# Performance work log

Hardware: AMD Instinct MI355X
Metric: run time of the kernel (lower is better)

Reference implementation:

```python
import jax, jax.numpy as jnp
import numpy as np

B, C, W, H = 8, 256, 64, 64


def _conv1x1(x, w, b):
    # 1x1 conv == per-pixel channel GEMM. x: [B,C,W,H], w: [O,C], b: [O]
    return jnp.einsum('oc,bchw->bohw', w, x) + b[None, :, None, None]


def setup_inputs() -> dict:
    key = jax.random.key(0)
    ks = jax.random.split(key, 9)
    s = 1.0 / np.sqrt(C)
    return {
        'queries': jax.random.normal(ks[0], (B, C, W, H), dtype=jnp.float32),
        'keys': jax.random.normal(ks[1], (B, C, W, H), dtype=jnp.float32),
        'mask': jax.random.uniform(ks[2], (B, 1, W, H), dtype=jnp.float32),
        'Wq': jax.random.normal(ks[3], (C, C), dtype=jnp.float32) * s,
        'bq': jax.random.normal(ks[4], (C,), dtype=jnp.float32) * 0.01,
        'Wk': jax.random.normal(ks[5], (C, C), dtype=jnp.float32) * s,
        'bk': jax.random.normal(ks[6], (C,), dtype=jnp.float32) * 0.01,
        'Wv': jax.random.normal(ks[7], (C, C), dtype=jnp.float32) * s,
        'bv': jax.random.normal(ks[8], (C,), dtype=jnp.float32) * 0.01,
    }


def reference(queries, keys, mask, Wq, bq, Wk, bk, Wv, bv):
    b, c, w, h = queries.shape
    n = w * h
    q = _conv1x1(queries, Wq, bq).reshape(b, c, n)   # [B,C,N]
    k = _conv1x1(keys, Wk, bk).reshape(b, c, n)      # [B,C,N]
    v = _conv1x1(keys, Wv, bv).reshape(b, c, n)      # [B,C,N]
    # mask spatial size equals feature size -> interpolate(scale_factor=1) is identity
    m = mask.reshape(b, n)                            # [B,N]
    # scores[b,i,j] = <q_i, k_j>; torch's repeated mask multiplies row i by mask[i]
    scores = jnp.einsum('bcq,bck->bqk', q, k) * m[:, :, None]
    attn_w = jax.nn.softmax(scores, axis=-1)          # softmax over key dim
    attn = jnp.einsum('bqk,bck->bcq', attn_w, v).reshape(b, c, w, h)
    return queries * mask + (1.0 - mask) * attn
```

## Files before the change

### kernel.cpp

```cpp
#include <hip/hip_runtime.h>

typedef __attribute__((ext_vector_type(8))) _Float16 half8;
typedef __attribute__((ext_vector_type(4))) _Float16 half4;
typedef __attribute__((ext_vector_type(4))) float f32x4;

#define CDIM 256
#define NDIM 4096
#define MFMAH(a, b, c) __builtin_amdgcn_mfma_f32_16x16x32_f16((a), (b), (c), 0, 0, 0)

#define GLOAD_LDS16(gp, lp)                                              \
  __builtin_amdgcn_global_load_lds(                                      \
      (const __attribute__((address_space(1))) void*)(gp),               \
      (__attribute__((address_space(3))) void*)(lp), 16, 0, 0)

__global__ void cast_w_kernel(const float* __restrict__ Wq,
                              const float* __restrict__ Wk,
                              const float* __restrict__ Wv,
                              _Float16* __restrict__ Wc) {
  int t = blockIdx.x * 256 + threadIdx.x;
  int mat = t >> 14;
  int idx = (t & 16383) * 4;
  const float* W = (mat == 0) ? Wq : (mat == 1 ? Wk : Wv);
  float4 w = *(const float4*)(W + idx);
  half4 h = {(_Float16)w.x, (_Float16)w.y, (_Float16)w.z, (_Float16)w.w};
  *(half4*)(Wc + mat * 65536 + idx) = h;
}

__global__ __launch_bounds__(256, 2) void proj_kernel(
    const float* __restrict__ queries, const float* __restrict__ keys,
    const _Float16* __restrict__ Wc,
    const float* __restrict__ bq, const float* __restrict__ bk,
    const float* __restrict__ bv,
    _Float16* __restrict__ Qh, _Float16* __restrict__ Kh,
    _Float16* __restrict__ Vh)
{
  const int z = blockIdx.z, p = z >> 3, b = z & 7;
  const float* __restrict__ X = (p == 0) ? queries : keys;
  const _Float16* __restrict__ W = Wc + p * 65536;
  const float* __restrict__ bias = (p == 0) ? bq : (p == 1 ? bk : bv);
  const int n0 = blockIdx.x * 128;

  __shared__ __align__(16) _Float16 Xs[128][264];

  const int tid = threadIdx.x;
  const int wv = tid >> 6, lane = tid & 63, l16 = lane & 15, quad = lane >> 4;

#pragma unroll
  for (int it = 0; it < 32; ++it) {
    int id = tid + it * 256;
    int c = id >> 5, n4 = id & 31;
    float4 x = *(const float4*)&X[((size_t)(b * CDIM + c)) * NDIM + n0 + n4 * 4];
    Xs[n4 * 4 + 0][c] = (_Float16)x.x;
    Xs[n4 * 4 + 1][c] = (_Float16)x.y;
    Xs[n4 * 4 + 2][c] = (_Float16)x.z;
    Xs[n4 * 4 + 3][c] = (_Float16)x.w;
  }
  __syncthreads();

  f32x4 acc[4][8];
#pragma unroll
  for (int og = 0; og < 4; ++og)
#pragma unroll
    for (int ng = 0; ng < 8; ++ng) acc[og][ng] = (f32x4){0.f, 0.f, 0.f, 0.f};

#pragma unroll
  for (int kc = 0; kc < 8; ++kc) {
    half8 wf[4], xf[8];
#pragma unroll
    for (int og = 0; og < 4; ++og)
      wf[og] = *(const half8*)(W + (wv * 64 + og * 16 + l16) * CDIM + kc * 32 + quad * 8);
#pragma unroll
    for (int ng = 0; ng < 8; ++ng)
      xf[ng] = *(const half8*)&Xs[ng * 16 + l16][kc * 32 + quad * 8];
#pragma unroll
    for (int og = 0; og < 4; ++og)
#pragma unroll
      for (int ng = 0; ng < 8; ++ng)
        acc[og][ng] = MFMAH(wf[og], xf[ng], acc[og][ng]);
  }

#pragma unroll
  for (int og = 0; og < 4; ++og) {
    float4 b4 = *(const float4*)&bias[wv * 64 + og * 16 + quad * 4];
#pragma unroll
    for (int ng = 0; ng < 8; ++ng) {
      const int n = n0 + ng * 16 + l16;
      if (p == 2) {
#pragma unroll
        for (int r = 0; r < 4; ++r) {
          int o = wv * 64 + og * 16 + quad * 4 + r;
          float y = acc[og][ng][r] + ((const float*)&b4)[r];
          Vh[((size_t)(b * CDIM + o)) * NDIM + n] = (_Float16)y;
        }
      } else {
        half4 h4;
#pragma unroll
        for (int r = 0; r < 4; ++r)
          h4[r] = (_Float16)(acc[og][ng][r] + ((const float*)&b4)[r]);
        size_t idx = ((size_t)(b * NDIM + n)) * CDIM + wv * 64 + og * 16 + quad * 4;
        if (p == 0) *(half4*)&Qh[idx] = h4;
        else        *(half4*)&Kh[idx] = h4;
      }
    }
  }
}

__global__ __launch_bounds__(256, 2) void attn_kernel(
    const float* __restrict__ queries, const float* __restrict__ mask,
    const _Float16* __restrict__ Qh, const _Float16* __restrict__ Kh,
    const _Float16* __restrict__ Vh, float* __restrict__ out)
{
  const int blk = blockIdx.x, b = blk & 7, it = blk >> 3;
  const int i0 = it * 64;

  __shared__ __align__(16) _Float16 Ks[64 * 256];
  __shared__ __align__(16) _Float16 Ps[2][64][88];
  __shared__ __align__(16) float Al[2][64];
  __shared__ __align__(16) float Li[64];

  const int tid = threadIdx.x;
  const int wv = tid >> 6, lane = tid & 63, l16 = lane & 15, quad = lane >> 4;

  const float LOG2E = 1.44269504088896f;

  half8 qf[8];
  {
    const size_t qrow = ((size_t)(b * NDIM + i0 + wv * 16 + l16)) * CDIM;
#pragma unroll
    for (int kc = 0; kc < 8; ++kc)
      qf[kc] = *(const half8*)(Qh + qrow + kc * 32 + quad * 8);
  }
  const float mvalL = mask[(size_t)b * NDIM + i0 + wv * 16 + l16] * LOG2E;
  float m_run = -1e30f, l_run = 0.f;

  f32x4 O[4][4];
#pragma unroll
  for (int g = 0; g < 4; ++g)
#pragma unroll
    for (int cg = 0; cg < 4; ++cg) O[g][cg] = (f32x4){0.f, 0.f, 0.f, 0.f};

  const _Float16* __restrict__ Kb = Kh + (size_t)b * NDIM * CDIM;
  const _Float16* __restrict__ Vw = Vh + ((size_t)(b * CDIM + wv * 64)) * NDIM;

  const int jrow = tid >> 5;
  const int scol = ((tid & 31) * 8) ^ ((jrow & 7) << 3);
  char* const ldst0 = (char*)Ks + (size_t)tid * 16;
  const int kswz = (l16 & 7) << 3;

#pragma unroll
  for (int st = 0; st < 8; ++st)
    GLOAD_LDS16(Kb + (size_t)(st * 8 + jrow) * CDIM + scol, ldst0 + st * 4096);

  for (int jt = 0; jt < 64; ++jt) {
    const int j0 = jt * 64;
    const int pb = jt & 1;
    half8 vf[2][4];
#pragma unroll
    for (int kk = 0; kk < 2; ++kk)
#pragma unroll
      for (int cg = 0; cg < 4; ++cg)
        vf[kk][cg] = *(const half8*)(Vw + (size_t)(cg * 16 + l16) * NDIM + j0 + kk * 32 + quad * 8);
    __syncthreads();

    f32x4 s[4];
#pragma unroll
    for (int js = 0; js < 4; ++js) s[js] = (f32x4){0.f, 0.f, 0.f, 0.f};
#pragma unroll
    for (int kc = 0; kc < 8; ++kc) {
#pragma unroll
      for (int js = 0; js < 4; ++js) {
        half8 kf = *(const half8*)&Ks[(js * 16 + l16) * 256 + ((kc * 32 + quad * 8) ^ kswz)];
        s[js] = MFMAH(kf, qf[kc], s[js]);
      }
    }

    float a[16];
    float mx = -1e30f;
#pragma unroll
    for (int js = 0; js < 4; ++js)
#pragma unroll
      for (int r = 0; r < 4; ++r) {
        float v = s[js][r] * mvalL;
        a[js * 4 + r] = v;
        mx = fmaxf(mx, v);
      }
    mx = fmaxf(mx, __shfl_xor(mx, 16));
    mx = fmaxf(mx, __shfl_xor(mx, 32));
    const float mnew = fmaxf(m_run, mx);
    const float alpha = exp2f(m_run - mnew);
    m_run = mnew;
    float psum = 0.f;
#pragma unroll
    for (int js = 0; js < 4; ++js) {
      float p0 = exp2f(a[js * 4 + 0] - mnew);
      float p1 = exp2f(a[js * 4 + 1] - mnew);
      float p2 = exp2f(a[js * 4 + 2] - mnew);
      float p3 = exp2f(a[js * 4 + 3] - mnew);
      psum += (p0 + p1) + (p2 + p3);
      half4 hp = {(_Float16)p0, (_Float16)p1, (_Float16)p2, (_Float16)p3};
      *(half4*)&Ps[pb][wv * 16 + l16][js * 16 + quad * 4] = hp;
    }
    psum += __shfl_xor(psum, 16);
    psum += __shfl_xor(psum, 32);
    l_run = l_run * alpha + psum;
    if (quad == 0) Al[pb][wv * 16 + l16] = alpha;
    __syncthreads();

    if (jt < 63) {
      const _Float16* srcn = Kb + (size_t)((jt + 1) * 64 + jrow) * CDIM + scol;
#pragma unroll
      for (int st = 0; st < 8; ++st)
        GLOAD_LDS16(srcn + (size_t)st * 8 * CDIM, ldst0 + st * 4096);
    }

    f32x4 av[4];
#pragma unroll
    for (int g = 0; g < 4; ++g) av[g] = *(const f32x4*)&Al[pb][g * 16 + quad * 4];
#pragma unroll
    for (int g = 0; g < 4; ++g)
#pragma unroll
      for (int cg = 0; cg < 4; ++cg)
#pragma unroll
        for (int r = 0; r < 4; ++r) O[g][cg][r] *= av[g][r];
#pragma unroll
    for (int kk = 0; kk < 2; ++kk) {
      half8 pa[4];
#pragma unroll
      for (int g = 0; g < 4; ++g)
        pa[g] = *(const half8*)&Ps[pb][g * 16 + l16][kk * 32 + quad * 8];
#pragma unroll
      for (int g = 0; g < 4; ++g)
#pragma unroll
        for (int cg = 0; cg < 4; ++cg)
          O[g][cg] = MFMAH(pa[g], vf[kk][cg], O[g][cg]);
    }
  }

  if (quad == 0) Li[wv * 16 + l16] = 1.0f / l_run;
  __syncthreads();
#pragma unroll
  for (int g = 0; g < 4; ++g) {
    f32x4 li4 = *(const f32x4*)&Li[g * 16 + quad * 4];
    const int i = i0 + g * 16 + quad * 4;
    float4 m4 = *(const float4*)&mask[(size_t)b * NDIM + i];
#pragma unroll
    for (int cg = 0; cg < 4; ++cg) {
      const int c = wv * 64 + cg * 16 + l16;
      const size_t base = ((size_t)(b * CDIM + c)) * NDIM + i;
      float4 q4 = *(const float4*)(queries + base);
      float4 o4;
      o4.x = q4.x * m4.x + (1.f - m4.x) * (O[g][cg][0] * li4[0]);
      o4.y = q4.y * m4.y + (1.f - m4.y) * (O[g][cg][1] * li4[1]);
      o4.z = q4.z * m4.z + (1.f - m4.z) * (O[g][cg][2] * li4[2]);
      o4.w = q4.w * m4.w + (1.f - m4.w) * (O[g][cg][3] * li4[3]);
      *(float4*)(out + base) = o4;
    }
  }
}

extern "C" void kernel_launch(void* const* d_in, const int* in_sizes, int n_in,
                              void* d_out, int out_size, void* d_ws, size_t ws_size,
                              hipStream_t stream) {
  const float* queries = (const float*)d_in[0];
  const float* keys    = (const float*)d_in[1];
  const float* mask    = (const float*)d_in[2];
  const float* Wq = (const float*)d_in[3];
  const float* bq = (const float*)d_in[4];
  const float* Wk = (const float*)d_in[5];
  const float* bk = (const float*)d_in[6];
  const float* Wv = (const float*)d_in[7];
  const float* bv = (const float*)d_in[8];
  float* out = (float*)d_out;

  const size_t elems = (size_t)8 * NDIM * CDIM;
  _Float16* Qh = (_Float16*)d_ws;
  _Float16* Kh = Qh + elems;
  _Float16* Vh = Kh + elems;
  _Float16* Wc = Vh + elems;

  cast_w_kernel<<<dim3(192), 256, 0, stream>>>(Wq, Wk, Wv, Wc);
  proj_kernel<<<dim3(32, 1, 24), 256, 0, stream>>>(
      queries, keys, Wc, bq, bk, bv, Qh, Kh, Vh);
  attn_kernel<<<dim3(512), 256, 0, stream>>>(
      queries, mask, Qh, Kh, Vh, out);
}
```

Before: 327.5 us.

## Split projection tile into two halves and prefetch second half into registers

The projection kernel now processes its 128-column tile as two 64-column halves. The second half's input is loaded into registers while the first half's MFMAs and stores run, then converted and written to a second LDS buffer. This is meant to overlap global-load latency with compute and to halve the accumulator register footprint. In exchange, each thread holds 16 float4 prefetch registers and the W fragments are reloaded for each half.

```diff
diff --git a/kernel.cpp b/kernel.cpp
--- a/kernel.cpp
+++ b/kernel.cpp
@@ -40,67 +40,91 @@
   const float* __restrict__ bias = (p == 0) ? bq : (p == 1 ? bk : bv);
   const int n0 = blockIdx.x * 128;
 
-  __shared__ __align__(16) _Float16 Xs[128][264];
+  __shared__ __align__(16) _Float16 Xs[2][64][264];
 
   const int tid = threadIdx.x;
   const int wv = tid >> 6, lane = tid & 63, l16 = lane & 15, quad = lane >> 4;
 
 #pragma unroll
-  for (int it = 0; it < 32; ++it) {
+  for (int it = 0; it < 16; ++it) {
     int id = tid + it * 256;
-    int c = id >> 5, n4 = id & 31;
+    int c = id >> 4, n4 = id & 15;
     float4 x = *(const float4*)&X[((size_t)(b * CDIM + c)) * NDIM + n0 + n4 * 4];
-    Xs[n4 * 4 + 0][c] = (_Float16)x.x;
-    Xs[n4 * 4 + 1][c] = (_Float16)x.y;
-    Xs[n4 * 4 + 2][c] = (_Float16)x.z;
-    Xs[n4 * 4 + 3][c] = (_Float16)x.w;
+    Xs[0][n4 * 4 + 0][c] = (_Float16)x.x;
+    Xs[0][n4 * 4 + 1][c] = (_Float16)x.y;
+    Xs[0][n4 * 4 + 2][c] = (_Float16)x.z;
+    Xs[0][n4 * 4 + 3][c] = (_Float16)x.w;
   }
   __syncthreads();
 
-  f32x4 acc[4][8];
-#pragma unroll
-  for (int og = 0; og < 4; ++og)
-#pragma unroll
-    for (int ng = 0; ng < 8; ++ng) acc[og][ng] = (f32x4){0.f, 0.f, 0.f, 0.f};
-
-#pragma unroll
-  for (int kc = 0; kc < 8; ++kc) {
-    half8 wf[4], xf[8];
+  float4 xs1[16];
+#pragma unroll
+  for (int it = 0; it < 16; ++it) {
+    int id = tid + it * 256;
+    int c = id >> 4, n4 = id & 15;
+    xs1[it] = *(const float4*)&X[((size_t)(b * CDIM + c)) * NDIM + n0 + 64 + n4 * 4];
+  }
+
+#pragma unroll
+  for (int s = 0; s < 2; ++s) {
+    f32x4 acc[4][4];
 #pragma unroll
     for (int og = 0; og < 4; ++og)
-      wf[og] = *(const half8*)(W + (wv * 64 + og * 16 + l16) * CDIM + kc * 32 + quad * 8);
-#pragma unroll
-    for (int ng = 0; ng < 8; ++ng)
-      xf[ng] = *(const half8*)&Xs[ng * 16 + l16][kc * 32 + quad * 8];
-#pragma unroll
-    for (int og = 0; og < 4; ++og)
-#pragma unroll
-      for (int ng = 0; ng < 8; ++ng)
-        acc[og][ng] = MFMAH(wf[og], xf[ng], acc[og][ng]);
-  }
-
-#pragma unroll
-  for (int og = 0; og < 4; ++og) {
-    float4 b4 = *(const float4*)&bias[wv * 64 + og * 16 + quad * 4];
-#pragma unroll
-    for (int ng = 0; ng < 8; ++ng) {
-      const int n = n0 + ng * 16 + l16;
-      if (p == 2) {
-#pragma unroll
-        for (int r = 0; r < 4; ++r) {
-          int o = wv * 64 + og * 16 + quad * 4 + r;
-          float y = acc[og][ng][r] + ((const float*)&b4)[r];
-          Vh[((size_t)(b * CDIM + o)) * NDIM + n] = (_Float16)y;
+#pragma unroll
+      for (int ng = 0; ng < 4; ++ng) acc[og][ng] = (f32x4){0.f, 0.f, 0.f, 0.f};
+
+#pragma unroll
+    for (int kc = 0; kc < 8; ++kc) {
+      half8 wf[4], xf[4];
+#pragma unroll
+      for (int og = 0; og < 4; ++og)
+        wf[og] = *(const half8*)(W + (wv * 64 + og * 16 + l16) * CDIM + kc * 32 + quad * 8);
+#pragma unroll
+      for (int ng = 0; ng < 4; ++ng)
+        xf[ng] = *(const half8*)&Xs[s][ng * 16 + l16][kc * 32 + quad * 8];
+#pragma unroll
+      for (int og = 0; og < 4; ++og)
+#pragma unroll
+        for (int ng = 0; ng < 4; ++ng)
+          acc[og][ng] = MFMAH(wf[og], xf[ng], acc[og][ng]);
+    }
+
+#pragma unroll
+    for (int og = 0; og < 4; ++og) {
+      float4 b4 = *(const float4*)&bias[wv * 64 + og * 16 + quad * 4];
+#pragma unroll
+      for (int ng = 0; ng < 4; ++ng) {
+        const int n = n0 + s * 64 + ng * 16 + l16;
+        if (p == 2) {
+#pragma unroll
+          for (int r = 0; r < 4; ++r) {
+            int o = wv * 64 + og * 16 + quad * 4 + r;
+            float y = acc[og][ng][r] + ((const float*)&b4)[r];
+            Vh[((size_t)(b * CDIM + o)) * NDIM + n] = (_Float16)y;
+          }
+        } else {
+          half4 h4;
+#pragma unroll
+          for (int r = 0; r < 4; ++r)
+            h4[r] = (_Float16)(acc[og][ng][r] + ((const float*)&b4)[r]);
+          size_t idx = ((size_t)(b * NDIM + n)) * CDIM + wv * 64 + og * 16 + quad * 4;
+          if (p == 0) *(half4*)&Qh[idx] = h4;
+          else        *(half4*)&Kh[idx] = h4;
         }
-      } else {
-        half4 h4;
-#pragma unroll
-        for (int r = 0; r < 4; ++r)
-          h4[r] = (_Float16)(acc[og][ng][r] + ((const float*)&b4)[r]);
-        size_t idx = ((size_t)(b * NDIM + n)) * CDIM + wv * 64 + og * 16 + quad * 4;
-        if (p == 0) *(half4*)&Qh[idx] = h4;
-        else        *(half4*)&Kh[idx] = h4;
       }
+    }
+
+    if (s == 0) {
+#pragma unroll
+      for (int it = 0; it < 16; ++it) {
+        int id = tid + it * 256;
+        int c = id >> 4, n4 = id & 15;
+        Xs[1][n4 * 4 + 0][c] = (_Float16)xs1[it].x;
+        Xs[1][n4 * 4 + 1][c] = (_Float16)xs1[it].y;
+        Xs[1][n4 * 4 + 2][c] = (_Float16)xs1[it].z;
+        Xs[1][n4 * 4 + 3][c] = (_Float16)xs1[it].w;
+      }
+      __syncthreads();
     }
   }
 }
```

After: 353.3 us. 1.08x slower.
